# Performance work log

Hardware: AMD Instinct MI355X
Metric: run time of the kernel (lower is better)

## Reference

```python
import jax, jax.numpy as jnp
import numpy as np

B, S, D, H, KVH = 1, 2048, 4096, 32, 8
HD = D // H  # head_dim = 128
ROPE_THETA = 500000.0
NEG_INF = -1e9


def setup_inputs() -> dict:
    key = jax.random.key(0)
    ks = jax.random.split(key, 5)
    x = jax.random.normal(ks[0], (B, S, D), jnp.float32)
    wq = jax.random.normal(ks[1], (D, H * HD), jnp.float32) * 0.02
    wk = jax.random.normal(ks[2], (D, KVH * HD), jnp.float32) * 0.02
    wv = jax.random.normal(ks[3], (D, KVH * HD), jnp.float32) * 0.02
    wo = jax.random.normal(ks[4], (H * HD, D), jnp.float32) * 0.02
    inv = 1.0 / (ROPE_THETA ** (np.arange(0, HD, 2, dtype=np.float32) / HD))
    ang = np.arange(S, dtype=np.float32)[:, None] * inv[None, :]  # [S, HD/2]
    return dict(x=x, wq=wq, wk=wk, wv=wv, wo=wo,
                freqs_cos=jnp.asarray(np.cos(ang)), freqs_sin=jnp.asarray(np.sin(ang)))


def _rope(t, cos, sin):
    # t: [B, S, h, HD]; complex rotation on even/odd interleaved pairs
    tr = t.reshape(*t.shape[:-1], HD // 2, 2)
    t0, t1 = tr[..., 0], tr[..., 1]
    c = cos[None, :, None, :]
    s = sin[None, :, None, :]
    o0 = t0 * c - t1 * s
    o1 = t0 * s + t1 * c
    return jnp.stack([o0, o1], axis=-1).reshape(t.shape)


def reference(x, wq, wk, wv, wo, freqs_cos, freqs_sin):
    # QKV projections (prefill path: seqlen>1, start_pos=0 -> causal flash attn)
    xq = (x @ wq).reshape(B, S, H, HD)
    xk = (x @ wk).reshape(B, S, KVH, HD)
    xv = (x @ wv).reshape(B, S, KVH, HD)
    xq = _rope(xq, freqs_cos, freqs_sin)
    xk = _rope(xk, freqs_cos, freqs_sin)
    # GQA: repeat kv heads to match query heads
    n_rep = H // KVH
    xk = jnp.repeat(xk, n_rep, axis=2)  # [B,S,H,HD]
    xv = jnp.repeat(xv, n_rep, axis=2)
    scale = 1.0 / jnp.sqrt(jnp.asarray(HD, xq.dtype))
    scores = jnp.einsum('bqhd,bkhd->bhqk', xq, xk) * scale
    causal = jnp.tril(jnp.ones((S, S), bool))
    scores = jnp.where(causal[None, None], scores, NEG_INF)
    probs = jax.nn.softmax(scores, axis=-1)
    out = jnp.einsum('bhqk,bkhd->bqhd', probs, xv)  # [B,S,H,HD]
    return out.reshape(B, S, H * HD) @ wo
```

## Files before the change

### kernel.cpp

```cpp
#include <hip/hip_runtime.h>
#include <type_traits>

typedef __attribute__((ext_vector_type(8))) short short8;
typedef __attribute__((ext_vector_type(4))) float float4v;

__device__ inline float bf2f(short s) {
    unsigned u = ((unsigned)(unsigned short)s) << 16;
    float f; __builtin_memcpy(&f, &u, 4); return f;
}
__device__ inline short f2bf(float f) {
    unsigned u; __builtin_memcpy(&u, &f, 4);
    unsigned lsb = (u >> 16) & 1;
    u += 0x7fffu + lsb;
    return (short)(u >> 16);
}

__device__ inline void glds16(const void* g, void* l) {
    __builtin_amdgcn_global_load_lds(
        (const __attribute__((address_space(1))) unsigned int*)g,
        (__attribute__((address_space(3))) unsigned int*)l, 16, 0, 0);
}

__global__ __launch_bounds__(256) void conv_f32_bf16(const float* __restrict__ in,
                                                     short* __restrict__ out, int n8) {
    int idx = blockIdx.x * 256 + threadIdx.x;
    if (idx >= n8) return;
    const float* src = in + (size_t)idx * 8;
    float4v a = *(const float4v*)src;
    float4v b = *(const float4v*)(src + 4);
    short8 o;
#pragma unroll
    for (int j = 0; j < 4; j++) { o[j] = f2bf(a[j]); o[4 + j] = f2bf(b[j]); }
    *(short8*)(out + (size_t)idx * 8) = o;
}

__global__ __launch_bounds__(256) void transpose_conv(const float* __restrict__ in,
                                                      short* __restrict__ out,
                                                      int K, int ldn, int noff) {
    __shared__ float t[64 * 65];
    const int n0 = blockIdx.x * 64, k0 = blockIdx.y * 64;
    const int tid = threadIdx.x;
#pragma unroll
    for (int i = 0; i < 4; i++) {
        int slot = tid + 256 * i;
        int row = slot >> 4, c4 = slot & 15;
        float4v v = *(const float4v*)(in + (size_t)(k0 + row) * ldn + noff + n0 + c4 * 4);
#pragma unroll
        for (int j = 0; j < 4; j++) t[row * 65 + c4 * 4 + j] = v[j];
    }
    __syncthreads();
#pragma unroll
    for (int i = 0; i < 2; i++) {
        int slot = tid + 256 * i;
        int row = slot >> 3, c8 = slot & 7;
        short8 v;
#pragma unroll
        for (int j = 0; j < 8; j++) v[j] = f2bf(t[(c8 * 8 + j) * 65 + row]);
        *(short8*)(out + (size_t)(n0 + row) * K + k0 + c8 * 8) = v;
    }
}

__global__ __launch_bounds__(256) void transpose_k(const short* __restrict__ in,
                                                   short* __restrict__ out,
                                                   int K, int N, int ldin) {
    __attribute__((aligned(16))) __shared__ short t[64 * 72];
    const int n0 = blockIdx.x * 64, k0 = blockIdx.y * 64;
    const int tid = threadIdx.x;
#pragma unroll
    for (int i = 0; i < 2; i++) {
        int slot = tid + 256 * i;
        int row = slot >> 3, c8 = slot & 7;
        *(short8*)&t[row * 72 + c8 * 8] =
            *(const short8*)(in + (size_t)(k0 + row) * ldin + n0 + c8 * 8);
    }
    __syncthreads();
#pragma unroll
    for (int i = 0; i < 2; i++) {
        int slot = tid + 256 * i;
        int row = slot >> 3, c8 = slot & 7;
        short8 v;
#pragma unroll
        for (int j = 0; j < 8; j++) v[j] = t[(c8 * 8 + j) * 72 + row];
        *(short8*)(out + (size_t)(n0 + row) * K + k0 + c8 * 8) = v;
    }
}

template <typename AT, typename CT>
__global__ __launch_bounds__(256) void gemm_bt_g(const AT* __restrict__ A,
                                                 const short* __restrict__ Bt,
                                                 CT* __restrict__ C,
                                                 int K, int ldc, int coff) {
    __attribute__((aligned(16))) __shared__ short As[128 * 64];
    __attribute__((aligned(16))) __shared__ short Bs[128 * 64];
    const int tid = threadIdx.x;
    const int lane = tid & 63, wave = tid >> 6;
    const int quad = lane >> 4, l16 = lane & 15;
    const int wr = wave >> 1, wc = wave & 1;
    const int m0 = blockIdx.y * 128, n0 = blockIdx.x * 128;
    const int lrow = lane >> 3, lc8 = lane & 7;

    float4v acc[4][4];
#pragma unroll
    for (int i = 0; i < 4; i++)
#pragma unroll
        for (int j = 0; j < 4; j++) acc[i][j] = (float4v){0.f, 0.f, 0.f, 0.f};

    for (int k0 = 0; k0 < K; k0 += 64) {
#pragma unroll
        for (int r = 0; r < 4; r++) {
            int slab = r * 4 + wave;
            glds16(Bt + (size_t)(n0 + slab * 8 + lrow) * K + k0 + lc8 * 8, &Bs[slab * 512]);
        }
        if constexpr (std::is_same<AT, short>::value) {
#pragma unroll
            for (int r = 0; r < 4; r++) {
                int slab = r * 4 + wave;
                glds16(A + (size_t)(m0 + slab * 8 + lrow) * K + k0 + lc8 * 8, &As[slab * 512]);
            }
        } else {
#pragma unroll
            for (int i = 0; i < 4; i++) {
                int slot = tid + 256 * i;
                int row = slot >> 3, c8 = slot & 7;
                const float* src = A + (size_t)(m0 + row) * K + k0 + c8 * 8;
                float4v a = *(const float4v*)src;
                float4v b = *(const float4v*)(src + 4);
                short8 o;
#pragma unroll
                for (int j = 0; j < 4; j++) { o[j] = f2bf(a[j]); o[4 + j] = f2bf(b[j]); }
                *(short8*)&As[row * 64 + c8 * 8] = o;
            }
        }
        __syncthreads();
#pragma unroll
        for (int kc = 0; kc < 2; kc++) {
            short8 afr[4], bfr[4];
#pragma unroll
            for (int rt = 0; rt < 4; rt++)
                afr[rt] = *(const short8*)&As[(wr * 64 + rt * 16 + l16) * 64 + kc * 32 + quad * 8];
#pragma unroll
            for (int ct = 0; ct < 4; ct++)
                bfr[ct] = *(const short8*)&Bs[(wc * 64 + ct * 16 + l16) * 64 + kc * 32 + quad * 8];
#pragma unroll
            for (int rt = 0; rt < 4; rt++)
#pragma unroll
                for (int ct = 0; ct < 4; ct++)
                    acc[rt][ct] = __builtin_amdgcn_mfma_f32_16x16x32_bf16(
                        afr[rt], bfr[ct], acc[rt][ct], 0, 0, 0);
        }
        __syncthreads();
    }
#pragma unroll
    for (int rt = 0; rt < 4; rt++)
#pragma unroll
        for (int ct = 0; ct < 4; ct++) {
            int col = coff + n0 + wc * 64 + ct * 16 + l16;
#pragma unroll
            for (int r = 0; r < 4; r++) {
                int row = m0 + wr * 64 + rt * 16 + quad * 4 + r;
                if constexpr (std::is_same<CT, float>::value)
                    C[(size_t)row * ldc + col] = acc[rt][ct][r];
                else
                    C[(size_t)row * ldc + col] = f2bf(acc[rt][ct][r]);
            }
        }
}

__global__ void rope_kernel(short* __restrict__ T, const float* __restrict__ cosb,
                            const float* __restrict__ sinb, int nheads, int ld) {
    int idx = blockIdx.x * 256 + threadIdx.x;
    int total = 2048 * nheads * 16;
    if (idx >= total) return;
    int chunk = idx & 15;
    int t2 = idx >> 4;
    int hh = t2 % nheads;
    int s = t2 / nheads;
    short* p = T + (size_t)s * ld + hh * 128 + chunk * 8;
    short8 v = *(short8*)p;
    short8 o;
#pragma unroll
    for (int t = 0; t < 4; t++) {
        int i = chunk * 4 + t;
        float c = cosb[s * 64 + i];
        float sn = sinb[s * 64 + i];
        float a = bf2f(v[2 * t]), b = bf2f(v[2 * t + 1]);
        o[2 * t] = f2bf(a * c - b * sn);
        o[2 * t + 1] = f2bf(a * sn + b * c);
    }
    *(short8*)p = o;
}

__global__ __launch_bounds__(256) void attn_kernel(const short* __restrict__ Q,
                                                   const short* __restrict__ K,
                                                   const short* __restrict__ Vt,
                                                   short* __restrict__ O, int ldk) {
    __attribute__((aligned(16))) __shared__ short Ks[64 * 128];
    __attribute__((aligned(16))) __shared__ short Vs[128 * 64];
    __attribute__((aligned(16))) __shared__ short Ps[4][16 * 72];
    const int tid = threadIdx.x;
    const int lane = tid & 63, wave = tid >> 6;
    const int quad = lane >> 4, l16 = lane & 15;
    const int h = blockIdx.y, kvh = h >> 2;
    const float scale = 0.08838834764831845f;

    for (int pass = 0; pass < 2; pass++) {
        const int qtile = pass ? (31 - (int)blockIdx.x) : (int)blockIdx.x;
        const int qbase = qtile * 64;
        const int q0 = qbase + wave * 16;
        const int nt = qtile + 1;

        short8 qf[4];
        const short* qrow = Q + (size_t)(q0 + l16) * 4096 + h * 128;
#pragma unroll
        for (int ks = 0; ks < 4; ks++) qf[ks] = *(const short8*)(qrow + ks * 32 + quad * 8);

        float4v o_acc[8];
#pragma unroll
        for (int i = 0; i < 8; i++) o_acc[i] = (float4v){0.f, 0.f, 0.f, 0.f};
        float m_i[4], l_i[4];
#pragma unroll
        for (int r = 0; r < 4; r++) { m_i[r] = -1e9f; l_i[r] = 0.f; }

        short8 kreg[4], vreg[4];
#pragma unroll
        for (int i = 0; i < 4; i++) {
            int slot = tid + 256 * i;
            int row = slot >> 4, c8 = slot & 15;
            kreg[i] = *(const short8*)(K + (size_t)row * ldk + kvh * 128 + c8 * 8);
        }
#pragma unroll
        for (int i = 0; i < 4; i++) {
            int slot = tid + 256 * i;
            int row = slot >> 3, c8 = slot & 7;
            vreg[i] = *(const short8*)(Vt + (size_t)(kvh * 128 + row) * 2048 + c8 * 8);
        }

        for (int t = 0; t < nt; t++) {
            const int kv0 = t * 64;
            __syncthreads();
#pragma unroll
            for (int i = 0; i < 4; i++) {
                int slot = tid + 256 * i;
                int row = slot >> 4, c8 = slot & 15;
                *(short8*)&Ks[row * 128 + ((c8 ^ (row & 15)) * 8)] = kreg[i];
            }
#pragma unroll
            for (int i = 0; i < 4; i++) {
                int slot = tid + 256 * i;
                int row = slot >> 3, c8 = slot & 7;
                *(short8*)&Vs[row * 64 + ((c8 ^ (row & 7)) * 8)] = vreg[i];
            }
            __syncthreads();
            if (t + 1 < nt) {
                const int kv1 = kv0 + 64;
#pragma unroll
                for (int i = 0; i < 4; i++) {
                    int slot = tid + 256 * i;
                    int row = slot >> 4, c8 = slot & 15;
                    kreg[i] = *(const short8*)(K + (size_t)(kv1 + row) * ldk + kvh * 128 + c8 * 8);
                }
#pragma unroll
                for (int i = 0; i < 4; i++) {
                    int slot = tid + 256 * i;
                    int row = slot >> 3, c8 = slot & 7;
                    vreg[i] = *(const short8*)(Vt + (size_t)(kvh * 128 + row) * 2048 + kv1 + c8 * 8);
                }
            }

            float4v s_acc[4];
#pragma unroll
            for (int i = 0; i < 4; i++) s_acc[i] = (float4v){0.f, 0.f, 0.f, 0.f};
            __builtin_amdgcn_s_setprio(1);
#pragma unroll
            for (int nsub = 0; nsub < 4; nsub++) {
                const int row = nsub * 16 + l16;
#pragma unroll
                for (int ks = 0; ks < 4; ks++) {
                    short8 kf = *(const short8*)&Ks[row * 128 + (((ks * 4 + quad) ^ l16) * 8)];
                    s_acc[nsub] = __builtin_amdgcn_mfma_f32_16x16x32_bf16(
                        qf[ks], kf, s_acc[nsub], 0, 0, 0);
                }
            }
            __builtin_amdgcn_s_setprio(0);

            const bool diag = (t == nt - 1);
            float p[4][4];
#pragma unroll
            for (int nsub = 0; nsub < 4; nsub++)
#pragma unroll
                for (int r = 0; r < 4; r++) {
                    float v = s_acc[nsub][r] * scale;
                    if (diag) {
                        int rowq = q0 + quad * 4 + r;
                        int col = kv0 + nsub * 16 + l16;
                        v = (col <= rowq) ? v : -1e9f;
                    }
                    p[nsub][r] = v;
                }
            float tm[4];
#pragma unroll
            for (int r = 0; r < 4; r++)
                tm[r] = fmaxf(fmaxf(p[0][r], p[1][r]), fmaxf(p[2][r], p[3][r]));
#pragma unroll
            for (int off = 1; off < 16; off <<= 1)
#pragma unroll
                for (int r = 0; r < 4; r++)
                    tm[r] = fmaxf(tm[r], __shfl_xor(tm[r], off, 64));
            float alpha[4], rs[4];
#pragma unroll
            for (int r = 0; r < 4; r++) {
                float mn = fmaxf(m_i[r], tm[r]);
                alpha[r] = __expf(m_i[r] - mn);
                m_i[r] = mn;
                rs[r] = 0.f;
            }
#pragma unroll
            for (int nsub = 0; nsub < 4; nsub++)
#pragma unroll
                for (int r = 0; r < 4; r++) {
                    float e = __expf(p[nsub][r] - m_i[r]);
                    rs[r] += e;
                    Ps[wave][(quad * 4 + r) * 72 + nsub * 16 + l16] = f2bf(e);
                }
#pragma unroll
            for (int off = 1; off < 16; off <<= 1)
#pragma unroll
                for (int r = 0; r < 4; r++) rs[r] += __shfl_xor(rs[r], off, 64);
#pragma unroll
            for (int r = 0; r < 4; r++) l_i[r] = l_i[r] * alpha[r] + rs[r];
#pragma unroll
            for (int dt = 0; dt < 8; dt++)
#pragma unroll
                for (int r = 0; r < 4; r++) o_acc[dt][r] *= alpha[r];

            short8 pf0 = *(const short8*)&Ps[wave][l16 * 72 + quad * 8];
            short8 pf1 = *(const short8*)&Ps[wave][l16 * 72 + 32 + quad * 8];
            __builtin_amdgcn_s_setprio(1);
#pragma unroll
            for (int dt = 0; dt < 8; dt++) {
                const int row = dt * 16 + l16;
                short8 vf0 = *(const short8*)&Vs[row * 64 + ((quad ^ (l16 & 7)) * 8)];
                short8 vf1 = *(const short8*)&Vs[row * 64 + (((4 + quad) ^ (l16 & 7)) * 8)];
                o_acc[dt] = __builtin_amdgcn_mfma_f32_16x16x32_bf16(pf0, vf0, o_acc[dt], 0, 0, 0);
                o_acc[dt] = __builtin_amdgcn_mfma_f32_16x16x32_bf16(pf1, vf1, o_acc[dt], 0, 0, 0);
            }
            __builtin_amdgcn_s_setprio(0);
        }

#pragma unroll
        for (int dt = 0; dt < 8; dt++)
#pragma unroll
            for (int r = 0; r < 4; r++) {
                int rowq = q0 + quad * 4 + r;
                O[(size_t)rowq * 4096 + h * 128 + dt * 16 + l16] = f2bf(o_acc[dt][r] / l_i[r]);
            }
    }
}

extern "C" void kernel_launch(void* const* d_in, const int* in_sizes, int n_in,
                              void* d_out, int out_size, void* d_ws, size_t ws_size,
                              hipStream_t stream) {
    (void)in_sizes; (void)n_in; (void)out_size;
    const float* x  = (const float*)d_in[0];
    const float* wq = (const float*)d_in[1];
    const float* wk = (const float*)d_in[2];
    const float* wv = (const float*)d_in[3];
    const float* wo = (const float*)d_in[4];
    const float* fc = (const float*)d_in[5];
    const float* fs = (const float*)d_in[6];
    float* out = (float*)d_out;
    char* ws = (char*)d_ws;
    const size_t MB = 1ull << 20;

    if (ws_size >= 76 * MB) {
        short* xb  = (short*)(ws);
        short* Qb  = (short*)(ws + 16 * MB);
        short* KVb = (short*)(ws + 32 * MB);
        short* Vt  = (short*)(ws + 40 * MB);
        short* WT  = (short*)(ws + 44 * MB);
        conv_f32_bf16<<<4096, 256, 0, stream>>>(x, xb, 2048 * 4096 / 8);
        transpose_conv<<<dim3(64, 64), 256, 0, stream>>>(wq, WT, 4096, 4096, 0);
        gemm_bt_g<short, short><<<dim3(32, 16), 256, 0, stream>>>(xb, WT, Qb, 4096, 4096, 0);
        transpose_conv<<<dim3(16, 64), 256, 0, stream>>>(wk, WT, 4096, 1024, 0);
        transpose_conv<<<dim3(16, 64), 256, 0, stream>>>(wv, WT + (size_t)1024 * 4096, 4096, 1024, 0);
        gemm_bt_g<short, short><<<dim3(16, 16), 256, 0, stream>>>(xb, WT, KVb, 4096, 2048, 0);
        rope_kernel<<<4096, 256, 0, stream>>>(Qb, fc, fs, 32, 4096);
        rope_kernel<<<1024, 256, 0, stream>>>(KVb, fc, fs, 8, 2048);
        transpose_k<<<dim3(16, 32), 256, 0, stream>>>(KVb + 1024, Vt, 2048, 1024, 2048);
        attn_kernel<<<dim3(16, 32), 256, 0, stream>>>(Qb, KVb, Vt, Qb, 2048);
        transpose_conv<<<dim3(64, 64), 256, 0, stream>>>(wo, WT, 4096, 4096, 0);
        gemm_bt_g<short, float><<<dim3(32, 16), 256, 0, stream>>>(Qb, WT, out, 4096, 4096, 0);
    } else if (ws_size >= 60 * MB) {
        short* xb  = (short*)(ws);
        short* Qb  = (short*)(ws + 16 * MB);
        short* KVb = (short*)(ws + 32 * MB);
        short* Vt  = (short*)(ws + 40 * MB);
        short* WT  = (short*)(ws + 44 * MB);
        conv_f32_bf16<<<4096, 256, 0, stream>>>(x, xb, 2048 * 4096 / 8);
        for (int s = 0; s < 2; s++) {
            transpose_conv<<<dim3(32, 64), 256, 0, stream>>>(wq, WT, 4096, 4096, s * 2048);
            gemm_bt_g<short, short><<<dim3(16, 16), 256, 0, stream>>>(xb, WT, Qb, 4096, 4096, s * 2048);
        }
        transpose_conv<<<dim3(16, 64), 256, 0, stream>>>(wk, WT, 4096, 1024, 0);
        transpose_conv<<<dim3(16, 64), 256, 0, stream>>>(wv, WT + (size_t)1024 * 4096, 4096, 1024, 0);
        gemm_bt_g<short, short><<<dim3(16, 16), 256, 0, stream>>>(xb, WT, KVb, 4096, 2048, 0);
        rope_kernel<<<4096, 256, 0, stream>>>(Qb, fc, fs, 32, 4096);
        rope_kernel<<<1024, 256, 0, stream>>>(KVb, fc, fs, 8, 2048);
        transpose_k<<<dim3(16, 32), 256, 0, stream>>>(KVb + 1024, Vt, 2048, 1024, 2048);
        attn_kernel<<<dim3(16, 32), 256, 0, stream>>>(Qb, KVb, Vt, Qb, 2048);
        for (int s = 0; s < 2; s++) {
            transpose_conv<<<dim3(32, 64), 256, 0, stream>>>(wo, WT, 4096, 4096, s * 2048);
            gemm_bt_g<short, float><<<dim3(16, 16), 256, 0, stream>>>(Qb, WT, out, 4096, 4096, s * 2048);
        }
    } else {
        short* WT = (short*)(ws);
        short* Qb = (short*)(ws + 8 * MB);
        short* Kb = (short*)(ws + 24 * MB);
        short* Vb = (short*)(ws + 28 * MB);
        short* Vt = (short*)(ws + 32 * MB);
        for (int s = 0; s < 4; s++) {
            transpose_conv<<<dim3(16, 64), 256, 0, stream>>>(wq, WT, 4096, 4096, s * 1024);
            gemm_bt_g<float, short><<<dim3(8, 16), 256, 0, stream>>>(x, WT, Qb, 4096, 4096, s * 1024);
        }
        transpose_conv<<<dim3(16, 64), 256, 0, stream>>>(wk, WT, 4096, 1024, 0);
        gemm_bt_g<float, short><<<dim3(8, 16), 256, 0, stream>>>(x, WT, Kb, 4096, 1024, 0);
        transpose_conv<<<dim3(16, 64), 256, 0, stream>>>(wv, WT, 4096, 1024, 0);
        gemm_bt_g<float, short><<<dim3(8, 16), 256, 0, stream>>>(x, WT, Vb, 4096, 1024, 0);
        rope_kernel<<<4096, 256, 0, stream>>>(Qb, fc, fs, 32, 4096);
        rope_kernel<<<1024, 256, 0, stream>>>(Kb, fc, fs, 8, 1024);
        transpose_k<<<dim3(16, 32), 256, 0, stream>>>(Vb, Vt, 2048, 1024, 1024);
        attn_kernel<<<dim3(16, 32), 256, 0, stream>>>(Qb, Kb, Vt, Qb, 1024);
        for (int s = 0; s < 4; s++) {
            transpose_conv<<<dim3(16, 64), 256, 0, stream>>>(wo, WT, 4096, 4096, s * 1024);
            gemm_bt_g<short, float><<<dim3(8, 16), 256, 0, stream>>>(Qb, WT, out, 4096, 4096, s * 1024);
        }
    }
}
```

Before: 597.3 us.

## Add 128x256-tile double-buffered GEMM with XOR swizzle for Q and O projections

```diff
diff --git a/kernel.cpp b/kernel.cpp
--- a/kernel.cpp
+++ b/kernel.cpp
@@ -83,6 +83,101 @@
         for (int j = 0; j < 8; j++) v[j] = t[(c8 * 8 + j) * 72 + row];
         *(short8*)(out + (size_t)(n0 + row) * K + k0 + c8 * 8) = v;
     }
+}
+
+template <typename CT>
+__global__ __launch_bounds__(512) void gemm_bt_p(const short* __restrict__ A,
+                                                 const short* __restrict__ Bt,
+                                                 CT* __restrict__ C) {
+    __attribute__((aligned(16))) __shared__ short lds[2][(128 + 256) * 64];
+    const int tid = threadIdx.x;
+    const int lane = tid & 63, wave = tid >> 6;
+    const int quad = lane >> 4, l16 = lane & 15;
+    const int wm = wave >> 2, wn = wave & 3;
+    const int b = blockIdx.x;
+    const int sw = (b & 7) * 32 + (b >> 3);
+    const int n0 = (sw & 15) * 256;
+    const int m0 = (sw >> 4) * 128;
+    const int lr = lane >> 3, lc = lane & 7;
+    const int swc = lc ^ lr;
+    const int K = 4096;
+
+    float4v acc[4][4];
+#pragma unroll
+    for (int i = 0; i < 4; i++)
+#pragma unroll
+        for (int j = 0; j < 4; j++) acc[i][j] = (float4v){0.f, 0.f, 0.f, 0.f};
+
+    auto stage = [&](int t, int buf) {
+        const int k0 = t * 64;
+        short* Ab = &lds[buf][0];
+        short* Bb = &lds[buf][128 * 64];
+#pragma unroll
+        for (int p = 0; p < 2; p++) {
+            int row = p * 64 + wave * 8;
+            glds16(A + (size_t)(m0 + row + lr) * K + k0 + swc * 8, Ab + row * 64);
+        }
+#pragma unroll
+        for (int p = 0; p < 4; p++) {
+            int row = p * 64 + wave * 8;
+            glds16(Bt + (size_t)(n0 + row + lr) * K + k0 + swc * 8, Bb + row * 64);
+        }
+    };
+
+    stage(0, 0);
+    stage(1, 1);
+
+    for (int t = 0; t < 64; t++) {
+        if (t + 1 < 64) asm volatile("s_waitcnt vmcnt(6)" ::: "memory");
+        else            asm volatile("s_waitcnt vmcnt(0)" ::: "memory");
+        __builtin_amdgcn_sched_barrier(0);
+        __builtin_amdgcn_s_barrier();
+        asm volatile("" ::: "memory");
+        const short* As = &lds[t & 1][0];
+        const short* Bs = &lds[t & 1][128 * 64];
+        short8 af[4][2], bf[4][2];
+#pragma unroll
+        for (int mf = 0; mf < 4; mf++)
+#pragma unroll
+            for (int kc = 0; kc < 2; kc++)
+                af[mf][kc] = *(const short8*)&As[(wm * 64 + mf * 16 + l16) * 64 +
+                                                 (((kc * 4 + quad) ^ (l16 & 7)) * 8)];
+#pragma unroll
+        for (int nf = 0; nf < 4; nf++)
+#pragma unroll
+            for (int kc = 0; kc < 2; kc++)
+                bf[nf][kc] = *(const short8*)&Bs[(wn * 64 + nf * 16 + l16) * 64 +
+                                                 (((kc * 4 + quad) ^ (l16 & 7)) * 8)];
+        __builtin_amdgcn_s_setprio(1);
+#pragma unroll
+        for (int mf = 0; mf < 4; mf++)
+#pragma unroll
+            for (int nf = 0; nf < 4; nf++)
+#pragma unroll
+                for (int kc = 0; kc < 2; kc++)
+                    acc[mf][nf] = __builtin_amdgcn_mfma_f32_16x16x32_bf16(
+                        af[mf][kc], bf[nf][kc], acc[mf][nf], 0, 0, 0);
+        __builtin_amdgcn_s_setprio(0);
+        asm volatile("" ::: "memory");
+        __builtin_amdgcn_s_barrier();
+        asm volatile("" ::: "memory");
+        if (t + 2 < 64) stage(t + 2, t & 1);
+    }
+
+#pragma unroll
+    for (int mf = 0; mf < 4; mf++)
+#pragma unroll
+        for (int nf = 0; nf < 4; nf++) {
+            int col = n0 + wn * 64 + nf * 16 + l16;
+#pragma unroll
+            for (int r = 0; r < 4; r++) {
+                int row = m0 + wm * 64 + mf * 16 + quad * 4 + r;
+                if constexpr (std::is_same<CT, float>::value)
+                    C[(size_t)row * 4096 + col] = acc[mf][nf][r];
+                else
+                    C[(size_t)row * 4096 + col] = f2bf(acc[mf][nf][r]);
+            }
+        }
 }
 
 template <typename AT, typename CT>
@@ -380,7 +475,7 @@
         short* WT  = (short*)(ws + 44 * MB);
         conv_f32_bf16<<<4096, 256, 0, stream>>>(x, xb, 2048 * 4096 / 8);
         transpose_conv<<<dim3(64, 64), 256, 0, stream>>>(wq, WT, 4096, 4096, 0);
-        gemm_bt_g<short, short><<<dim3(32, 16), 256, 0, stream>>>(xb, WT, Qb, 4096, 4096, 0);
+        gemm_bt_p<short><<<256, 512, 0, stream>>>(xb, WT, Qb);
         transpose_conv<<<dim3(16, 64), 256, 0, stream>>>(wk, WT, 4096, 1024, 0);
         transpose_conv<<<dim3(16, 64), 256, 0, stream>>>(wv, WT + (size_t)1024 * 4096, 4096, 1024, 0);
         gemm_bt_g<short, short><<<dim3(16, 16), 256, 0, stream>>>(xb, WT, KVb, 4096, 2048, 0);
@@ -389,7 +484,7 @@
         transpose_k<<<dim3(16, 32), 256, 0, stream>>>(KVb + 1024, Vt, 2048, 1024, 2048);
         attn_kernel<<<dim3(16, 32), 256, 0, stream>>>(Qb, KVb, Vt, Qb, 2048);
         transpose_conv<<<dim3(64, 64), 256, 0, stream>>>(wo, WT, 4096, 4096, 0);
-        gemm_bt_g<short, float><<<dim3(32, 16), 256, 0, stream>>>(Qb, WT, out, 4096, 4096, 0);
+        gemm_bt_p<float><<<256, 512, 0, stream>>>(Qb, WT, out);
     } else if (ws_size >= 60 * MB) {
         short* xb  = (short*)(ws);
         short* Qb  = (short*)(ws + 16 * MB);
```

Result: faster. 542.2 us (-9.2%).
